# Optimization experiments

Hardware: AMD Instinct MI355X
Metric: run time of the kernel (lower is better)

## Reference

```python
import jax, jax.numpy as jnp
import numpy as np

B, S, H, NH = 16, 1024, 512, 8
DH = H // NH
EPS = 1e-12
COV_MIN = 1e-24


def _split_heads(x):
    b, s, _ = x.shape
    return x.reshape(b, s, NH, DH).transpose(0, 2, 1, 3)  # [B,NH,S,DH]


def _merge_heads(x):
    b, nh, s, dh = x.shape
    return x.transpose(0, 2, 1, 3).reshape(b, s, nh * dh)


def _layernorm(x, w, b):
    u = jnp.mean(x, -1, keepdims=True)
    s = jnp.mean((x - u) ** 2, -1, keepdims=True)
    return w * ((x - u) / jnp.sqrt(s + EPS)) + b


def _wasserstein(mq, cq, mk, ck):
    # mean part: ||mq_i - mk_j||^2 via matmul expansion
    ret = (-2.0 * jnp.einsum('bhid,bhjd->bhij', mq, mk)
           + jnp.sum(mq ** 2, -1)[..., :, None]
           + jnp.sum(mk ** 2, -1)[..., None, :])
    sq_cq = jnp.sqrt(jnp.clip(cq, COV_MIN))
    sq_ck = jnp.sqrt(jnp.clip(ck, COV_MIN))
    cov_ret = (-2.0 * jnp.einsum('bhid,bhjd->bhij', sq_cq, sq_ck)
               + jnp.sum(cq, -1)[..., :, None]
               + jnp.sum(ck, -1)[..., None, :])
    return ret + cov_ret


def setup_inputs() -> dict:
    key = jax.random.key(0)
    ks = jax.random.split(key, 16)
    d = {
        'x_mean': jax.random.normal(ks[0], (B, S, H), jnp.float32),
        'x_resp_mean': jax.random.normal(ks[1], (B, S, H), jnp.float32),
        'x_cov': jax.random.normal(ks[2], (B, S, H), jnp.float32),
        'x_resp_cov': jax.random.normal(ks[3], (B, S, H), jnp.float32),
    }
    causal = jnp.tril(jnp.ones((S, S), bool))
    d['attn_mask'] = jnp.where(causal, 0.0, -1e4).astype(jnp.float32)[None, None]
    names = ['mq', 'mk', 'mv', 'cq', 'ck', 'cv', 'md', 'cd']
    for i, n in enumerate(names):
        d[n + '_w'] = jax.random.normal(ks[4 + i], (H, H), jnp.float32) * 0.02
        d[n + '_b'] = jnp.zeros((H,), jnp.float32)
    d['ln_w'] = jnp.ones((H,), jnp.float32)
    d['ln_b'] = jnp.zeros((H,), jnp.float32)
    return d


def reference(x_mean, x_resp_mean, x_cov, x_resp_cov, attn_mask,
              mq_w, mq_b, mk_w, mk_b, mv_w, mv_b,
              cq_w, cq_b, ck_w, ck_b, cv_w, cv_b,
              md_w, md_b, cd_w, cd_b, ln_w, ln_b):
    mq = _split_heads(x_mean @ mq_w + mq_b)
    mk = _split_heads(x_mean @ mk_w + mk_b)
    mv = _split_heads(x_resp_mean @ mv_w + mv_b)
    cq = _split_heads(jax.nn.elu(x_cov @ cq_w + cq_b) + 1.0)
    ck = _split_heads(jax.nn.elu(x_cov @ ck_w + ck_b) + 1.0)
    cv = _split_heads(jax.nn.elu(x_resp_cov @ cv_w + cv_b) + 1.0)

    scores = -_wasserstein(mq, cq, mk, ck) / np.sqrt(DH).astype(np.float32)
    scores = scores + attn_mask
    probs = jax.nn.softmax(scores, axis=-1)  # [B,NH,S,S]
    # zero_pad=True: zero out the first query row
    probs = probs.at[:, :, 0, :].set(0.0)

    mean_ctx = _merge_heads(jnp.einsum('bhij,bhjd->bhid', probs, mv))
    cov_ctx = _merge_heads(jnp.einsum('bhij,bhjd->bhid', probs ** 2, cv))

    mean_h = _layernorm(mean_ctx @ md_w + md_b + x_mean, ln_w, ln_b)
    cov_h = _layernorm(cov_ctx @ cd_w + cd_b + x_cov, ln_w, ln_b)
    return mean_h, cov_h, probs
```

## Files before the change

### kernel.cpp

```cpp
#include <hip/hip_runtime.h>
#include <math.h>

#define SLEN 1024
#define NH 8
#define DH 64
#define HDIM 512
#define BATCH 16
#define NROWS (BATCH * SLEN)
#define BHN (BATCH * NH)
#define BHROWS (BHN * SLEN)

typedef short bf16x8 __attribute__((ext_vector_type(8)));
typedef unsigned short u16x8 __attribute__((ext_vector_type(8)));
typedef float f32x4 __attribute__((ext_vector_type(4)));

__device__ __forceinline__ unsigned short f2bf(float f) {
    unsigned u = __float_as_uint(f);
    u += 0x7fffu + ((u >> 16) & 1u);
    return (unsigned short)(u >> 16);
}
__device__ __forceinline__ float bf2f(unsigned short h) {
    return __uint_as_float(((unsigned)h) << 16);
}

struct Args {
    const float *xm, *xrm, *xc, *xrc;
    const float *w[8], *bias[8];
    const float *ln_w, *ln_b;
    unsigned short *xbf, *wt;
    float *sums;
    unsigned short *qcat, *kcat, *vcat, *vcat_t, *ctxm, *ctxc;
    float *out_m, *out_c, *probs;
};

__global__ void __launch_bounds__(256) cvt_inputs_k(Args P) {
    const int which = blockIdx.y;
    const float *s = which == 0 ? P.xm : which == 1 ? P.xrm : which == 2 ? P.xc : P.xrc;
    unsigned short *d = P.xbf + (size_t)which * 8388608;
    const long long i = ((long long)blockIdx.x * 256 + threadIdx.x) * 8;
    if (i >= 8388608) return;
    float4 a = *(const float4 *)(s + i);
    float4 b = *(const float4 *)(s + i + 4);
    u16x8 o;
    o[0] = f2bf(a.x); o[1] = f2bf(a.y); o[2] = f2bf(a.z); o[3] = f2bf(a.w);
    o[4] = f2bf(b.x); o[5] = f2bf(b.y); o[6] = f2bf(b.z); o[7] = f2bf(b.w);
    *(u16x8 *)(d + i) = o;
}

__global__ void __launch_bounds__(256) wtrans_k(Args P) {
    const int op = blockIdx.y;
    const float *W = P.w[op];
    unsigned short *WT = P.wt + (size_t)op * 262144;
    const int kt = blockIdx.x >> 3, nt = blockIdx.x & 7;
    __shared__ float Ws[64][65];
    const int t = threadIdx.x;
#pragma unroll
    for (int it = 0; it < 4; ++it) {
        int g = t + 256 * it;
        int k = g >> 4, n4 = (g & 15) * 4;
        float4 v = *(const float4 *)(W + (size_t)(kt * 64 + k) * 512 + nt * 64 + n4);
        Ws[k][n4] = v.x; Ws[k][n4 + 1] = v.y; Ws[k][n4 + 2] = v.z; Ws[k][n4 + 3] = v.w;
    }
    __syncthreads();
#pragma unroll
    for (int it = 0; it < 2; ++it) {
        int g = t + 256 * it;
        int n = g >> 3, kg = (g & 7) * 8;
        u16x8 o;
#pragma unroll
        for (int e = 0; e < 8; ++e) o[e] = f2bf(Ws[kg + e][n]);
        *(u16x8 *)(WT + (size_t)(nt * 64 + n) * 512 + kt * 64 + kg) = o;
    }
}

__global__ void __launch_bounds__(256) mgemm0_k(Args P) {
    const int op = blockIdx.z;
    const int srcidx[6] = {0, 0, 1, 2, 2, 3};
    const unsigned short *Abf = P.xbf + (size_t)srcidx[op] * 8388608;
    const unsigned short *WT = P.wt + (size_t)op * 262144;
    const float *bias = P.bias[op];
    unsigned short *dstb; int doff, act;
    switch (op) {
        case 0: dstb = P.qcat; doff = 0;  act = 0; break;
        case 1: dstb = P.kcat; doff = 0;  act = 0; break;
        case 2: dstb = P.vcat; doff = 0;  act = 0; break;
        case 3: dstb = P.qcat; doff = 64; act = 1; break;
        case 4: dstb = P.kcat; doff = 64; act = 1; break;
        default:dstb = P.vcat; doff = 64; act = 2; break;
    }
    const int lin = blockIdx.y * 4 + blockIdx.x;
    const int xcd = lin & 7, idx = lin >> 3;
    const int m0 = (xcd * 16 + (idx >> 2)) * 128;
    const int n0 = (idx & 3) * 128;

    __shared__ unsigned short As[128][64];
    __shared__ unsigned short Bs[128][64];
    const int t = threadIdx.x;
    const int wid = t >> 6, lane = t & 63;
    const int wm = wid >> 1, wn = wid & 1;
    const int l16 = lane & 15, lq = lane >> 4;

    f32x4 acc[4][4];
#pragma unroll
    for (int i = 0; i < 4; ++i)
#pragma unroll
        for (int j = 0; j < 4; ++j) acc[i][j] = (f32x4)(0.f);

    for (int k0 = 0; k0 < 512; k0 += 64) {
        __syncthreads();
#pragma unroll
        for (int it = 0; it < 4; ++it) {
            int g = t + 256 * it;
            int r = g >> 3, cg = g & 7;
            bf16x8 av = *(const bf16x8 *)(Abf + (size_t)(m0 + r) * 512 + k0 + cg * 8);
            *(bf16x8 *)&As[r][(cg ^ (r & 7)) * 8] = av;
            bf16x8 bv = *(const bf16x8 *)(WT + (size_t)(n0 + r) * 512 + k0 + cg * 8);
            *(bf16x8 *)&Bs[r][(cg ^ (r & 7)) * 8] = bv;
        }
        __syncthreads();
#pragma unroll
        for (int kk = 0; kk < 2; ++kk) {
            bf16x8 a[4], b[4];
#pragma unroll
            for (int mf = 0; mf < 4; ++mf) {
                int r = wm * 64 + mf * 16 + l16;
                int cg = kk * 4 + lq;
                a[mf] = *(const bf16x8 *)&As[r][(cg ^ (r & 7)) * 8];
            }
#pragma unroll
            for (int nf = 0; nf < 4; ++nf) {
                int r = wn * 64 + nf * 16 + l16;
                int cg = kk * 4 + lq;
                b[nf] = *(const bf16x8 *)&Bs[r][(cg ^ (r & 7)) * 8];
            }
#pragma unroll
            for (int mf = 0; mf < 4; ++mf)
#pragma unroll
                for (int nf = 0; nf < 4; ++nf)
                    acc[mf][nf] = __builtin_amdgcn_mfma_f32_16x16x32_bf16(a[mf], b[nf], acc[mf][nf], 0, 0, 0);
        }
    }

#pragma unroll
    for (int mf = 0; mf < 4; ++mf) {
#pragma unroll
        for (int nf = 0; nf < 4; ++nf) {
#pragma unroll
            for (int r = 0; r < 4; ++r) {
                const int i = m0 + wm * 64 + mf * 16 + lq * 4 + r;
                const int j = n0 + wn * 64 + nf * 16 + l16;
                float v = acc[mf][nf][r] + bias[j];
                if (act == 1) {
                    float e = v > 0.f ? v + 1.f : expf(v);
                    v = sqrtf(fmaxf(e, 1e-24f));
                } else if (act == 2) {
                    v = v > 0.f ? v + 1.f : expf(v);
                }
                const int b_ = i >> 10, s_ = i & (SLEN - 1);
                const int h_ = j >> 6, d_ = j & (DH - 1);
                dstb[((size_t)(b_ * NH + h_) * SLEN + s_) * 128 + doff + d_] = f2bf(v);
            }
        }
    }
}

__global__ void __launch_bounds__(256) vtrans_k(Args P) {
    const int bh = blockIdx.y;
    const int s0 = blockIdx.x * 128;
    __shared__ unsigned short Ts[128][136];
    const unsigned short *src = P.vcat + (size_t)bh * SLEN * 128;
    unsigned short *dst = P.vcat_t + (size_t)bh * 128 * SLEN;
    const int t = threadIdx.x;
#pragma unroll
    for (int it = 0; it < 8; ++it) {
        int g = t + 256 * it;
        int s = g >> 4, dg = g & 15;
        *(u16x8 *)&Ts[s][dg * 8] = *(const u16x8 *)(src + (size_t)(s0 + s) * 128 + dg * 8);
    }
    __syncthreads();
#pragma unroll
    for (int it = 0; it < 8; ++it) {
        int g = t + 256 * it;
        int d = g >> 4, sg = g & 15;
        u16x8 o;
#pragma unroll
        for (int e = 0; e < 8; ++e) o[e] = Ts[sg * 8 + e][d];
        *(u16x8 *)(dst + (size_t)d * SLEN + s0 + sg * 8) = o;
    }
}

__global__ void __launch_bounds__(256) rowsum_k(Args P) {
    const int t = threadIdx.x;
    const int wv = t >> 6, lane = t & 63;
    const long long row = (long long)blockIdx.x * 4 + wv;
    const unsigned short *src = (row < BHROWS) ? P.qcat : P.kcat;
    const long long r = row & (BHROWS - 1);
    const unsigned short *p = src + r * 128;
    float a = bf2f(p[lane]), b = bf2f(p[64 + lane]);
    float v = a * a + b * b;
#pragma unroll
    for (int o = 32; o > 0; o >>= 1) v += __shfl_xor(v, o);
    if (lane == 0) P.sums[row] = v;
}

__global__ void __launch_bounds__(1024, 4) flash_k(Args P) {
    const int bh = blockIdx.x;
    const int qt = 15 - (int)blockIdx.y;
    const int q0 = qt * 64;
    __shared__ unsigned short Ep[64][1024];
    __shared__ unsigned short Ks[64][128];
    __shared__ float Tred[4][64];
    __shared__ float Tsh[64];
    unsigned short (*Vt)[64] = reinterpret_cast<unsigned short (*)[64]>(&Ks[0][0]);

    const int t = threadIdx.x;
    const int w = t >> 6, lane = t & 63;
    const int l16 = lane & 15, lq = lane >> 4;
    const int mg = w >> 2, q4 = w & 3;

    const unsigned short *qc = P.qcat + (size_t)bh * SLEN * 128;
    const unsigned short *kc = P.kcat + (size_t)bh * SLEN * 128;
    const float *qsum = P.sums + (size_t)bh * SLEN;
    const float *ksum = P.sums + BHROWS + (size_t)bh * SLEN;

    const unsigned short *qrow = qc + (size_t)(q0 + mg * 16 + l16) * 128;
    bf16x8 qfr[4];
#pragma unroll
    for (int kk = 0; kk < 4; ++kk) qfr[kk] = *(const bf16x8 *)(qrow + (kk * 4 + lq) * 8);
    float qs[4];
#pragma unroll
    for (int r = 0; r < 4; ++r) qs[r] = qsum[q0 + mg * 16 + lq * 4 + r];

    const int nkt = qt + 1;
    float tpart[4] = {0.f, 0.f, 0.f, 0.f};

    for (int kt = 0; kt < nkt; ++kt) {
        const int k0 = kt * 64;
        __syncthreads();
        {
            int r = t >> 4, g = t & 15;
            *(bf16x8 *)&Ks[r][(g ^ (r & 7)) * 8] =
                *(const bf16x8 *)(kc + (size_t)(k0 + r) * 128 + g * 8);
        }
        __syncthreads();

        const int rK = q4 * 16 + l16;
        const float ksv = ksum[k0 + rK];
        f32x4 acc = (f32x4)(0.f);
#pragma unroll
        for (int kk = 0; kk < 4; ++kk) {
            bf16x8 b = *(const bf16x8 *)&Ks[rK][((kk * 4 + lq) ^ (rK & 7)) * 8];
            acc = __builtin_amdgcn_mfma_f32_16x16x32_bf16(qfr[kk], b, acc, 0, 0, 0);
        }
        const int j = k0 + rK;
#pragma unroll
        for (int r = 0; r < 4; ++r) {
            const int row = mg * 16 + lq * 4 + r;
            const int i = q0 + row;
            float sv = (2.f * acc[r] - qs[r] - ksv) * 0.125f;
            float e = (j <= i) ? __expf(sv) : 0.f;
            tpart[r] += e;
            Ep[row][(((j >> 3) ^ (row & 7)) << 3) | (j & 7)] = f2bf(e);
        }
    }

#pragma unroll
    for (int o = 1; o < 16; o <<= 1)
#pragma unroll
        for (int r = 0; r < 4; ++r) tpart[r] += __shfl_xor(tpart[r], o);
    if (l16 == 0) {
#pragma unroll
        for (int r = 0; r < 4; ++r) Tred[q4][mg * 16 + lq * 4 + r] = tpart[r];
    }
    __syncthreads();
    if (t < 64) {
        const int i = q0 + t;
        const float T = Tred[0][t] + Tred[1][t] + Tred[2][t] + Tred[3][t];
        Tsh[t] = (i == 0) ? 0.f : (1.f / T);
    }
    __syncthreads();

    {
        float *pout = P.probs + ((size_t)bh * SLEN + q0) * SLEN;
#pragma unroll
        for (int it = 0; it < 8; ++it) {
            const int row = it * 8 + (t >> 7);
            const int c0 = (t & 127) * 8;
            const int i = q0 + row;
            const float inv = Tsh[row];
            const int g = c0 >> 3;
            u16x8 v = *(const u16x8 *)&Ep[row][((g ^ (row & 7)) << 3)];
            f32x4 o0, o1;
#pragma unroll
            for (int e = 0; e < 4; ++e)
                o0[e] = (c0 + e <= i) ? bf2f(v[e]) * inv : 0.f;
#pragma unroll
            for (int e = 0; e < 4; ++e)
                o1[e] = (c0 + 4 + e <= i) ? bf2f(v[4 + e]) * inv : 0.f;
            f32x4 *dst = (f32x4 *)(pout + (size_t)row * SLEN + c0);
            dst[0] = o0;
            dst[1] = o1;
        }
    }

    const int cov = q4 >> 1;
    f32x4 pacc[2];
    pacc[0] = (f32x4)(0.f); pacc[1] = (f32x4)(0.f);
    const unsigned short *vtg = P.vcat_t + (size_t)bh * 128 * SLEN;
    for (int kt = 0; kt < nkt; ++kt) {
        const int k0 = kt * 64;
        __syncthreads();
        {
            int d = t >> 3, g = t & 7;
            *(bf16x8 *)&Vt[d][(g ^ (d & 7)) * 8] =
                *(const bf16x8 *)(vtg + (size_t)d * SLEN + k0 + g * 8);
        }
        __syncthreads();
#pragma unroll
        for (int kk = 0; kk < 2; ++kk) {
            const int row = mg * 16 + l16;
            const int gg = (k0 >> 3) + kk * 4 + lq;
            bf16x8 af = *(const bf16x8 *)&Ep[row][((gg ^ (row & 7)) << 3)];
            if (cov) {
                u16x8 u = (u16x8)af, sq;
#pragma unroll
                for (int e = 0; e < 8; ++e) {
                    float f = bf2f(u[e]);
                    sq[e] = f2bf(f * f);
                }
                af = (bf16x8)sq;
            }
#pragma unroll
            for (int nf = 0; nf < 2; ++nf) {
                const int d = q4 * 32 + nf * 16 + l16;
                bf16x8 bf = *(const bf16x8 *)&Vt[d][((kk * 4 + lq) ^ (d & 7)) * 8];
                pacc[nf] = __builtin_amdgcn_mfma_f32_16x16x32_bf16(af, bf, pacc[nf], 0, 0, 0);
            }
        }
    }

    unsigned short *dst = cov ? P.ctxc : P.ctxm;
    const int b_ = bh >> 3, h_ = bh & 7;
#pragma unroll
    for (int nf = 0; nf < 2; ++nf) {
#pragma unroll
        for (int r = 0; r < 4; ++r) {
            const int row = mg * 16 + lq * 4 + r;
            const int s_ = q0 + row;
            const float inv = Tsh[row];
            const float scale = cov ? inv * inv : inv;
            dst[((size_t)b_ * SLEN + s_) * HDIM + h_ * 64 + (q4 & 1) * 32 + nf * 16 + l16] =
                f2bf(pacc[nf][r] * scale);
        }
    }
}

__global__ void __launch_bounds__(512, 4) mgemm_ln_k(Args P) {
    const int op = blockIdx.y;
    const unsigned short *Abf = op ? P.ctxc : P.ctxm;
    const unsigned short *WT = P.wt + (size_t)(6 + op) * 262144;
    const float *bias = P.bias[6 + op];
    const float *resid = op ? P.xc : P.xm;
    float *out = op ? P.out_c : P.out_m;
    const int m0 = blockIdx.x * 64;

    __shared__ unsigned short As[64][64];
    __shared__ unsigned short Bs[512][64];
    __shared__ float Red[64][4][2];

    const int t = threadIdx.x;
    const int w = t >> 6, lane = t & 63;
    const int wm = w >> 2, wn = w & 3;
    const int l16 = lane & 15, lq = lane >> 4;

    f32x4 acc[2][8];
#pragma unroll
    for (int mf = 0; mf < 2; ++mf)
#pragma unroll
        for (int nf = 0; nf < 8; ++nf) acc[mf][nf] = (f32x4)(0.f);

    for (int k0 = 0; k0 < 512; k0 += 64) {
        __syncthreads();
        {
            int r = t >> 3, cg = t & 7;
            *(bf16x8 *)&As[r][(cg ^ (r & 7)) * 8] =
                *(const bf16x8 *)(Abf + (size_t)(m0 + r) * 512 + k0 + cg * 8);
        }
#pragma unroll
        for (int it = 0; it < 8; ++it) {
            int g = t + 512 * it;
            int r = g >> 3, cg = g & 7;
            *(bf16x8 *)&Bs[r][(cg ^ (r & 7)) * 8] =
                *(const bf16x8 *)(WT + (size_t)r * 512 + k0 + cg * 8);
        }
        __syncthreads();
#pragma unroll
        for (int kk = 0; kk < 2; ++kk) {
            bf16x8 a[2];
#pragma unroll
            for (int mf = 0; mf < 2; ++mf) {
                int r = wm * 32 + mf * 16 + l16;
                a[mf] = *(const bf16x8 *)&As[r][((kk * 4 + lq) ^ (r & 7)) * 8];
            }
#pragma unroll
            for (int nf = 0; nf < 8; ++nf) {
                int rn = wn * 128 + nf * 16 + l16;
                bf16x8 b = *(const bf16x8 *)&Bs[rn][((kk * 4 + lq) ^ (rn & 7)) * 8];
#pragma unroll
                for (int mf = 0; mf < 2; ++mf)
                    acc[mf][nf] = __builtin_amdgcn_mfma_f32_16x16x32_bf16(a[mf], b, acc[mf][nf], 0, 0, 0);
            }
        }
    }

    float bv[8];
#pragma unroll
    for (int nf = 0; nf < 8; ++nf) bv[nf] = bias[wn * 128 + nf * 16 + l16];

    float s0[2][4], s1[2][4];
#pragma unroll
    for (int mf = 0; mf < 2; ++mf)
#pragma unroll
        for (int r = 0; r < 4; ++r) { s0[mf][r] = 0.f; s1[mf][r] = 0.f; }

#pragma unroll
    for (int mf = 0; mf < 2; ++mf) {
#pragma unroll
        for (int r = 0; r < 4; ++r) {
            const int i = m0 + wm * 32 + mf * 16 + lq * 4 + r;
            const float *rrow = resid + (size_t)i * HDIM + wn * 128 + l16;
#pragma unroll
            for (int nf = 0; nf < 8; ++nf) {
                float x = acc[mf][nf][r] + bv[nf] + rrow[nf * 16];
                acc[mf][nf][r] = x;
                s0[mf][r] += x;
                s1[mf][r] += x * x;
            }
        }
    }
#pragma unroll
    for (int o = 1; o < 16; o <<= 1)
#pragma unroll
        for (int mf = 0; mf < 2; ++mf)
#pragma unroll
            for (int r = 0; r < 4; ++r) {
                s0[mf][r] += __shfl_xor(s0[mf][r], o);
                s1[mf][r] += __shfl_xor(s1[mf][r], o);
            }
    if (l16 == 0) {
#pragma unroll
        for (int mf = 0; mf < 2; ++mf)
#pragma unroll
            for (int r = 0; r < 4; ++r) {
                const int row = wm * 32 + mf * 16 + lq * 4 + r;
                Red[row][wn][0] = s0[mf][r];
                Red[row][wn][1] = s1[mf][r];
            }
    }
    __syncthreads();

    float lnw[8], lnb[8];
#pragma unroll
    for (int nf = 0; nf < 8; ++nf) {
        const int j = wn * 128 + nf * 16 + l16;
        lnw[nf] = P.ln_w[j]; lnb[nf] = P.ln_b[j];
    }
#pragma unroll
    for (int mf = 0; mf < 2; ++mf) {
#pragma unroll
        for (int r = 0; r < 4; ++r) {
            const int row = wm * 32 + mf * 16 + lq * 4 + r;
            const int i = m0 + row;
            const float S  = Red[row][0][0] + Red[row][1][0] + Red[row][2][0] + Red[row][3][0];
            const float SS = Red[row][0][1] + Red[row][1][1] + Red[row][2][1] + Red[row][3][1];
            const float mean = S * (1.f / 512.f);
            const float var = SS * (1.f / 512.f) - mean * mean;
            const float inv = 1.f / sqrtf(var + 1e-12f);
            float *orow = out + (size_t)i * HDIM + wn * 128 + l16;
#pragma unroll
            for (int nf = 0; nf < 8; ++nf)
                orow[nf * 16] = lnw[nf] * ((acc[mf][nf][r] - mean) * inv) + lnb[nf];
        }
    }
}

extern "C" void kernel_launch(void *const *d_in, const int *in_sizes, int n_in,
                              void *d_out, int out_size, void *d_ws, size_t ws_size,
                              hipStream_t stream) {
    (void)in_sizes; (void)n_in; (void)out_size; (void)ws_size;
    Args P;
    P.xm  = (const float *)d_in[0];
    P.xrm = (const float *)d_in[1];
    P.xc  = (const float *)d_in[2];
    P.xrc = (const float *)d_in[3];
    for (int i = 0; i < 8; ++i) {
        P.w[i]    = (const float *)d_in[5 + 2 * i];
        P.bias[i] = (const float *)d_in[6 + 2 * i];
    }
    P.ln_w = (const float *)d_in[21];
    P.ln_b = (const float *)d_in[22];

    char *ws = (char *)d_ws;
    P.xbf    = (unsigned short *)(ws);
    P.vcat_t = (unsigned short *)(ws);
    P.ctxm   = (unsigned short *)(ws + 33554432);
    P.ctxc   = (unsigned short *)(ws + 50331648);
    P.wt     = (unsigned short *)(ws + 67108864);
    P.sums   = (float *)(ws + 71303168);
    P.qcat   = (unsigned short *)(ws + 72351744);
    P.kcat   = (unsigned short *)(ws + 105906176);
    P.vcat   = (unsigned short *)(ws + 139460608);

    P.out_m = (float *)d_out;
    P.out_c = (float *)d_out + 8388608;
    P.probs = (float *)d_out + 16777216;

    cvt_inputs_k<<<dim3(4096, 4), dim3(256), 0, stream>>>(P);
    wtrans_k<<<dim3(64, 8), dim3(256), 0, stream>>>(P);
    mgemm0_k<<<dim3(4, 128, 6), dim3(256), 0, stream>>>(P);
    vtrans_k<<<dim3(8, 128), dim3(256), 0, stream>>>(P);
    rowsum_k<<<dim3(65536), dim3(256), 0, stream>>>(P);
    flash_k<<<dim3(128, 16), dim3(1024), 0, stream>>>(P);
    mgemm_ln_k<<<dim3(256, 2), dim3(512), 0, stream>>>(P);
}
```

Before: 540.3 us.

## Register-prefetch K/V tiles and interleave probs writes with PV loop

Loads the next K and V tiles into registers while the current tile is computed, so global loads overlap the MFMA work instead of sitting between two barriers. The probs output write is split up: the masked upper region is zeroed early, and each 64-column block of normalized probabilities is stored inside the PV loop, mixing stores with compute. Reading Ep in the PV loop with a narrower per-thread pattern may add shared-memory traffic, and the extra live registers could lower occupancy.

After: 485.2 us. 1.11x faster.

```diff
diff --git a/kernel.cpp b/kernel.cpp
--- a/kernel.cpp
+++ b/kernel.cpp
@@ -222,6 +222,7 @@
     const unsigned short *kc = P.kcat + (size_t)bh * SLEN * 128;
     const float *qsum = P.sums + (size_t)bh * SLEN;
     const float *ksum = P.sums + BHROWS + (size_t)bh * SLEN;
+    float *pout = P.probs + ((size_t)bh * SLEN + q0) * SLEN;
 
     const unsigned short *qrow = qc + (size_t)(q0 + mg * 16 + l16) * 128;
     bf16x8 qfr[4];
@@ -234,25 +235,28 @@
     const int nkt = qt + 1;
     float tpart[4] = {0.f, 0.f, 0.f, 0.f};
 
+    const int sr = t >> 4, sg = t & 15;
+    const int rK = q4 * 16 + l16;
+    bf16x8 kreg = *(const bf16x8 *)(kc + (size_t)sr * 128 + sg * 8);
+    float ksreg = ksum[rK];
+
     for (int kt = 0; kt < nkt; ++kt) {
-        const int k0 = kt * 64;
-        __syncthreads();
-        {
-            int r = t >> 4, g = t & 15;
-            *(bf16x8 *)&Ks[r][(g ^ (r & 7)) * 8] =
-                *(const bf16x8 *)(kc + (size_t)(k0 + r) * 128 + g * 8);
-        }
-        __syncthreads();
-
-        const int rK = q4 * 16 + l16;
-        const float ksv = ksum[k0 + rK];
+        __syncthreads();
+        *(bf16x8 *)&Ks[sr][(sg ^ (sr & 7)) * 8] = kreg;
+        if (kt + 1 < nkt)
+            kreg = *(const bf16x8 *)(kc + (size_t)((kt + 1) * 64 + sr) * 128 + sg * 8);
+        __syncthreads();
+
+        const float ksv = ksreg;
+        if (kt + 1 < nkt) ksreg = ksum[(kt + 1) * 64 + rK];
+
         f32x4 acc = (f32x4)(0.f);
 #pragma unroll
         for (int kk = 0; kk < 4; ++kk) {
             bf16x8 b = *(const bf16x8 *)&Ks[rK][((kk * 4 + lq) ^ (rK & 7)) * 8];
             acc = __builtin_amdgcn_mfma_f32_16x16x32_bf16(qfr[kk], b, acc, 0, 0, 0);
         }
-        const int j = k0 + rK;
+        const int j = kt * 64 + rK;
 #pragma unroll
         for (int r = 0; r < 4; ++r) {
             const int row = mg * 16 + lq * 4 + r;
@@ -264,6 +268,16 @@
         }
     }
 
+    const int vr = t >> 3, vg = t & 7;
+    const unsigned short *vtg = P.vcat_t + (size_t)bh * 128 * SLEN;
+    bf16x8 vreg = *(const bf16x8 *)(vtg + (size_t)vr * SLEN + vg * 8);
+    {
+        const int zrow = t >> 4;
+        f32x4 z = (f32x4)(0.f);
+        for (int c4 = nkt * 16 + (t & 15); c4 < 256; c4 += 16)
+            *(f32x4 *)(pout + (size_t)zrow * SLEN + c4 * 4) = z;
+    }
+
 #pragma unroll
     for (int o = 1; o < 16; o <<= 1)
 #pragma unroll
@@ -280,46 +294,20 @@
     }
     __syncthreads();
 
-    {
-        float *pout = P.probs + ((size_t)bh * SLEN + q0) * SLEN;
-#pragma unroll
-        for (int it = 0; it < 8; ++it) {
-            const int row = it * 8 + (t >> 7);
-            const int c0 = (t & 127) * 8;
-            const int i = q0 + row;
-            const float inv = Tsh[row];
-            const int g = c0 >> 3;
-            u16x8 v = *(const u16x8 *)&Ep[row][((g ^ (row & 7)) << 3)];
-            f32x4 o0, o1;
-#pragma unroll
-            for (int e = 0; e < 4; ++e)
-                o0[e] = (c0 + e <= i) ? bf2f(v[e]) * inv : 0.f;
-#pragma unroll
-            for (int e = 0; e < 4; ++e)
-                o1[e] = (c0 + 4 + e <= i) ? bf2f(v[4 + e]) * inv : 0.f;
-            f32x4 *dst = (f32x4 *)(pout + (size_t)row * SLEN + c0);
-            dst[0] = o0;
-            dst[1] = o1;
-        }
-    }
-
     const int cov = q4 >> 1;
     f32x4 pacc[2];
     pacc[0] = (f32x4)(0.f); pacc[1] = (f32x4)(0.f);
-    const unsigned short *vtg = P.vcat_t + (size_t)bh * 128 * SLEN;
     for (int kt = 0; kt < nkt; ++kt) {
-        const int k0 = kt * 64;
-        __syncthreads();
-        {
-            int d = t >> 3, g = t & 7;
-            *(bf16x8 *)&Vt[d][(g ^ (d & 7)) * 8] =
-                *(const bf16x8 *)(vtg + (size_t)d * SLEN + k0 + g * 8);
-        }
-        __syncthreads();
+        __syncthreads();
+        *(bf16x8 *)&Vt[vr][(vg ^ (vr & 7)) * 8] = vreg;
+        if (kt + 1 < nkt)
+            vreg = *(const bf16x8 *)(vtg + (size_t)vr * SLEN + (kt + 1) * 64 + vg * 8);
+        __syncthreads();
+
 #pragma unroll
         for (int kk = 0; kk < 2; ++kk) {
             const int row = mg * 16 + l16;
-            const int gg = (k0 >> 3) + kk * 4 + lq;
+            const int gg = (kt * 8) + kk * 4 + lq;
             bf16x8 af = *(const bf16x8 *)&Ep[row][((gg ^ (row & 7)) << 3)];
             if (cov) {
                 u16x8 u = (u16x8)af, sq;
@@ -336,6 +324,26 @@
                 bf16x8 bf = *(const bf16x8 *)&Vt[d][((kk * 4 + lq) ^ (d & 7)) * 8];
                 pacc[nf] = __builtin_amdgcn_mfma_f32_16x16x32_bf16(af, bf, pacc[nf], 0, 0, 0);
             }
+        }
+
+        {
+            const int prow = t >> 4, slot = t & 15;
+            const int col = kt * 64 + slot * 4;
+            const int g = col >> 3, o4 = (slot & 1) * 4;
+            u16x8 v = *(const u16x8 *)&Ep[prow][((g ^ (prow & 7)) << 3)];
+            const float inv = Tsh[prow];
+            f32x4 ov;
+            if (kt == qt) {
+                const int i = q0 + prow;
+#pragma unroll
+                for (int e = 0; e < 4; ++e)
+                    ov[e] = (col + e <= i) ? bf2f(v[o4 + e]) * inv : 0.f;
+            } else {
+#pragma unroll
+                for (int e = 0; e < 4; ++e)
+                    ov[e] = bf2f(v[o4 + e]) * inv;
+            }
+            *(f32x4 *)(pout + (size_t)prow * SLEN + col) = ov;
         }
     }
 
```
